# Kernel optimization log

Hardware: AMD Instinct MI355X
Metric: run time of the kernel (lower is better)

The kernel has to match this reference:

```python
import jax, jax.numpy as jnp
import numpy as np

B, N = 32, 512
NODE_F, EDGE_F = 64, 16
OUT = [64, 64, 64, 128]
TARGET = 16
DEGS = [1, 2, 3, 4]  # degree buckets (degree 0 filtered out, as in init_duvenaud)


def setup_inputs() -> dict:
    key = jax.random.key(0)
    ks = jax.random.split(key, 12)
    # adjacency: each node v connects to v+1..v+deg(v) (mod N), deg in {1..4}
    deg = jax.random.randint(ks[0], (B, N), 1, 5)
    off = jnp.arange(1, 5)                                   # (4,)
    cols = (jnp.arange(N)[:, None] + off[None, :]) % N       # (N,4)
    vals = (off[None, None, :] <= deg[:, :, None]).astype(jnp.float32)  # (B,N,4)
    g = jnp.zeros((B, N, N), jnp.float32).at[:, jnp.arange(N)[:, None], cols].set(vals)
    h_in = jax.random.normal(ks[1], (B, N, NODE_F), jnp.float32)
    e = jax.random.normal(ks[2], (B, N, N, EDGE_F), jnp.float32)
    # per-timestep, per-degree update matrices H_t: (n_deg, msg_in_t, out_t)
    ins = [NODE_F + EDGE_F, OUT[0] + EDGE_F, OUT[1] + EDGE_F]
    H0 = jax.random.normal(ks[3], (len(DEGS), ins[0], OUT[0]), jnp.float32)
    H1 = jax.random.normal(ks[4], (len(DEGS), ins[1], OUT[1]), jnp.float32)
    H2 = jax.random.normal(ks[5], (len(DEGS), ins[2], OUT[2]), jnp.float32)
    # readout matrices W_l for each of the 4 stored layers h^0..h^3
    layer_in = [NODE_F, OUT[0], OUT[1], OUT[2]]
    W0 = jax.random.normal(ks[6], (layer_in[0], OUT[3]), jnp.float32)
    W1 = jax.random.normal(ks[7], (layer_in[1], OUT[3]), jnp.float32)
    W2 = jax.random.normal(ks[8], (layer_in[2], OUT[3]), jnp.float32)
    W3 = jax.random.normal(ks[9], (layer_in[3], OUT[3]), jnp.float32)
    W_final = jax.random.normal(ks[10], (OUT[3], TARGET), jnp.float32) * 0.05
    b_final = jnp.zeros((TARGET,), jnp.float32)
    return {"g": g, "h_in": h_in, "e": e,
            "H0": H0, "H1": H1, "H2": H2,
            "W0": W0, "W1": W1, "W2": W2, "W3": W3,
            "W_final": W_final, "b_final": b_final}


def _step(g, e, h, H):
    # duvenaud message m_v = sum_w g[v,w] * cat(h_w, e_vw); split concat to avoid
    # materializing the (B,N,N,F+E) tensor the torch loop builds per node.
    mh = jnp.einsum('bvw,bwf->bvf', g, h)
    me = jnp.einsum('bvw,bvwe->bve', g, e)
    m = jnp.concatenate([mh, me], axis=-1)                 # (B,N,msg_in)
    deg = jnp.sum(g, axis=2)                               # (B,N) node degrees
    # degree-bucketed linear update: h'_v = m_v @ H[bucket(deg_v)]
    cand = jnp.einsum('bvm,dmo->bvdo', m, H)               # (B,N,n_deg,out)
    degs = jnp.asarray(DEGS, m.dtype)
    sel = (deg[:, :, None] == degs[None, None, :]).astype(m.dtype)  # one-hot bucket
    return jnp.einsum('bvd,bvdo->bvo', sel, cand)          # deg not in DEGS -> 0


def reference(g, h_in, e, H0, H1, H2, W0, W1, W2, W3, W_final, b_final):
    hs = [h_in]
    for H in (H0, H1, H2):
        hs.append(_step(g, e, hs[-1], H))
    # duvenaud readout: sum over layers/nodes of masked softmax(h_l @ W_l)
    acc = jnp.zeros((g.shape[0], W_final.shape[0]), h_in.dtype)
    for h, W in zip(hs, (W0, W1, W2, W3)):
        lin = jnp.einsum('bvf,fo->bvo', h, W)
        # mask rows whose linear output is all zero (padding / never-updated nodes)
        mask = (jnp.sum(lin != 0, axis=-1, keepdims=True) > 0).astype(lin.dtype)
        acc = acc + jnp.sum(jax.nn.softmax(lin, axis=-1) * mask, axis=1)
    out = acc @ W_final + b_final
    return jax.nn.softmax(out, axis=-1)
```

## Files before the change

kernel.cpp:

```cpp
#include <hip/hip_runtime.h>

#define BATCH 32
#define NN 512
#define NODE_F 64
#define EDGE_F 16
#define MSG 80
#define OUTF 64
#define RD 128
#define TGT 16
#define KMAX 8
#define ROWS (BATCH*NN)

__global__ __launch_bounds__(256) void preprocess_kernel(
    const float* __restrict__ g, const float* __restrict__ e,
    int* __restrict__ adj_idx, float* __restrict__ adj_val,
    int* __restrict__ nnzArr, int* __restrict__ bucketArr,
    float* __restrict__ me)
{
  __shared__ int   s_idx[4][KMAX];
  __shared__ float s_val[4][KMAX];
  int lane = threadIdx.x & 63;
  int wid  = threadIdx.x >> 6;
  int row  = blockIdx.x * 4 + wid;
  const float* grow = g + (size_t)row * NN;
  float deg = 0.f;
  int cnt = 0;
  for (int it = 0; it < NN/64; ++it) {
    int w = it*64 + lane;
    float gv = grow[w];
    deg += gv;
    unsigned long long m = __ballot(gv != 0.0f);
    int before = __popcll(m & ((1ull << lane) - 1ull));
    if (gv != 0.0f) {
      int pos = cnt + before;
      if (pos < KMAX) { s_idx[wid][pos] = w; s_val[wid][pos] = gv; }
    }
    cnt += __popcll(m);
  }
  for (int off = 32; off; off >>= 1) deg += __shfl_xor(deg, off);
  __syncthreads();
  const float* erow = e + (size_t)row * NN * EDGE_F;
  float mef = 0.f;
  if (cnt <= KMAX) {
    for (int k = 0; k < cnt; ++k) {
      int   wk = s_idx[wid][k];
      float vk = s_val[wid][k];
      if (lane < EDGE_F) mef += vk * erow[wk*EDGE_F + lane];
    }
  } else {
    for (int w = 0; w < NN; ++w) {
      float gv = grow[w];
      if (gv != 0.f && lane < EDGE_F) mef += gv * erow[w*EDGE_F + lane];
    }
  }
  if (lane < EDGE_F) me[(size_t)row*EDGE_F + lane] = mef;
  if (lane < KMAX && lane < cnt) {
    adj_idx[row*KMAX + lane] = s_idx[wid][lane];
    adj_val[row*KMAX + lane] = s_val[wid][lane];
  }
  if (lane == 0) {
    int bk = -1;
    if      (deg == 1.0f) bk = 0;
    else if (deg == 2.0f) bk = 1;
    else if (deg == 3.0f) bk = 2;
    else if (deg == 4.0f) bk = 3;
    bucketArr[row] = bk;
    nnzArr[row] = cnt;
  }
}

__global__ void scatter_kernel(const int* __restrict__ bucketArr,
                               int* __restrict__ counts, int* __restrict__ perm)
{
  int i = blockIdx.x * blockDim.x + threadIdx.x;
  if (i < ROWS) {
    int bk = bucketArr[i];
    if (bk >= 0) {
      int p = atomicAdd(&counts[bk], 1);
      perm[bk*ROWS + p] = i;
    }
  }
}

__global__ __launch_bounds__(256) void step_kernel(
    const float* __restrict__ h_prev, float* __restrict__ h_out,
    const float* __restrict__ Ht,
    const int* __restrict__ perm, const int* __restrict__ counts,
    const int* __restrict__ nnzArr, const int* __restrict__ adj_idx,
    const float* __restrict__ adj_val, const float* __restrict__ me,
    const float* __restrict__ g)
{
  int d = blockIdx.x >> 10;
  int chunk = blockIdx.x & 1023;
  int cnt = counts[d];
  int base = chunk * 16;
  if (base >= cnt) return;
  __shared__ float sm[16][MSG];
  __shared__ int   srow[16];
  int lane = threadIdx.x & 63;
  int wid  = threadIdx.x >> 6;
  for (int j = 0; j < 4; ++j) {
    int nl = wid + 4*j;
    int gi = base + nl;
    if (gi < cnt) {
      int row = perm[d*ROWS + gi];
      if (lane == 0) srow[nl] = row;
      int bb  = row >> 9;
      int nnz = nnzArr[row];
      float mh = 0.f;
      if (nnz <= KMAX) {
        for (int k = 0; k < nnz; ++k) {
          int   w  = adj_idx[row*KMAX + k];
          float vv = adj_val[row*KMAX + k];
          mh += vv * h_prev[((size_t)(bb*NN + w))*NODE_F + lane];
        }
      } else {
        const float* grow = g + (size_t)row * NN;
        for (int w = 0; w < NN; ++w) {
          float gv = grow[w];
          if (gv != 0.f) mh += gv * h_prev[((size_t)(bb*NN + w))*NODE_F + lane];
        }
      }
      sm[nl][lane] = mh;
      if (lane < EDGE_F) sm[nl][NODE_F + lane] = me[(size_t)row*EDGE_F + lane];
    } else {
      if (lane == 0) srow[nl] = -1;
      sm[nl][lane] = 0.f;
      if (lane < EDGE_F) sm[nl][NODE_F + lane] = 0.f;
    }
  }
  __syncthreads();
  const float* Hd = Ht + d * MSG * OUTF;
  int o = lane, q = wid;
  float a0=0.f, a1=0.f, a2=0.f, a3=0.f;
  for (int i = 0; i < MSG; ++i) {
    float hv = Hd[i*OUTF + o];
    a0 += sm[q   ][i]*hv;
    a1 += sm[q+ 4][i]*hv;
    a2 += sm[q+ 8][i]*hv;
    a3 += sm[q+12][i]*hv;
  }
  float av[4] = {a0,a1,a2,a3};
  for (int j = 0; j < 4; ++j) {
    int r = srow[q + 4*j];
    if (r >= 0) h_out[(size_t)r*OUTF + o] = av[j];
  }
}

__global__ __launch_bounds__(128) void readout_kernel(
    const float* __restrict__ h0, const float* __restrict__ h1,
    const float* __restrict__ h2, const float* __restrict__ h3,
    const float* __restrict__ W0, const float* __restrict__ W1,
    const float* __restrict__ W2, const float* __restrict__ W3,
    float* __restrict__ accv)
{
  int l = blockIdx.x >> 9;
  int chunk = blockIdx.x & 511;
  const float* hs = (l==0)?h0:(l==1)?h1:(l==2)?h2:h3;
  const float* Wl = (l==0)?W0:(l==1)?W1:(l==2)?W2:W3;
  __shared__ float sW[NODE_F*RD];
  __shared__ float sh[32*NODE_F];
  __shared__ float sred[2], sred2[2];
  __shared__ int   sflag[2];
  int tid = threadIdx.x;
  const float4* W4 = (const float4*)Wl;
  float4* sW4 = (float4*)sW;
  for (int i = tid; i < NODE_F*RD/4; i += 128) sW4[i] = W4[i];
  const float4* h4 = (const float4*)(hs + (size_t)chunk*32*NODE_F);
  float4* sh4 = (float4*)sh;
  for (int i = tid; i < 32*NODE_F/4; i += 128) sh4[i] = h4[i];
  __syncthreads();
  int o = tid, wid = tid >> 6, lane = tid & 63;
  int b = chunk >> 4;
  float accl = 0.f;
  for (int n = 0; n < 32; ++n) {
    float lin = 0.f;
    for (int i = 0; i < NODE_F; ++i) lin += sh[n*NODE_F+i] * sW[i*RD+o];
    float mx = lin;
    for (int off = 32; off; off >>= 1) mx = fmaxf(mx, __shfl_xor(mx, off));
    int anyw = (__ballot(lin != 0.f) != 0ull) ? 1 : 0;
    if (lane == 0) { sred[wid] = mx; sflag[wid] = anyw; }
    __syncthreads();
    mx = fmaxf(sred[0], sred[1]);
    int any = sflag[0] | sflag[1];
    float p = expf(lin - mx);
    float s = p;
    for (int off = 32; off; off >>= 1) s += __shfl_xor(s, off);
    if (lane == 0) sred2[wid] = s;
    __syncthreads();
    s = sred2[0] + sred2[1];
    if (any) accl += p / s;
    __syncthreads();
  }
  atomicAdd(&accv[b*RD + o], accl);
}

__global__ __launch_bounds__(512) void final_kernel(
    const float* __restrict__ accv, const float* __restrict__ Wf,
    const float* __restrict__ bf, float* __restrict__ out)
{
  int tid = threadIdx.x;
  int b = tid >> 4, t = tid & 15;
  float v = bf[t];
  for (int i = 0; i < RD; ++i) v += accv[b*RD + i] * Wf[i*TGT + t];
  float mx = v;
  for (int off = 8; off; off >>= 1) mx = fmaxf(mx, __shfl_xor(mx, off, 16));
  float p = expf(v - mx);
  float s = p;
  for (int off = 8; off; off >>= 1) s += __shfl_xor(s, off, 16);
  out[tid] = p / s;
}

extern "C" void kernel_launch(void* const* d_in, const int* in_sizes, int n_in,
                              void* d_out, int out_size, void* d_ws, size_t ws_size,
                              hipStream_t stream)
{
  const float* g    = (const float*)d_in[0];
  const float* h_in = (const float*)d_in[1];
  const float* e    = (const float*)d_in[2];
  const float* H0   = (const float*)d_in[3];
  const float* H1   = (const float*)d_in[4];
  const float* H2   = (const float*)d_in[5];
  const float* W0   = (const float*)d_in[6];
  const float* W1   = (const float*)d_in[7];
  const float* W2   = (const float*)d_in[8];
  const float* W3   = (const float*)d_in[9];
  const float* Wf   = (const float*)d_in[10];
  const float* bf   = (const float*)d_in[11];
  float* out = (float*)d_out;

  char* base = (char*)d_ws;
  size_t off = 0;
  auto alloc = [&](size_t bytes) -> void* {
    void* p = base + off;
    off = (off + bytes + 255) & ~(size_t)255;
    return p;
  };
  int*   adj_idx   = (int*)  alloc((size_t)ROWS*KMAX*sizeof(int));
  float* adj_val   = (float*)alloc((size_t)ROWS*KMAX*sizeof(float));
  int*   nnzArr    = (int*)  alloc((size_t)ROWS*sizeof(int));
  int*   bucketArr = (int*)  alloc((size_t)ROWS*sizeof(int));
  float* me        = (float*)alloc((size_t)ROWS*EDGE_F*sizeof(float));
  int*   perm      = (int*)  alloc((size_t)4*ROWS*sizeof(int));
  int*   counts    = (int*)  alloc(4*sizeof(int) + (size_t)BATCH*RD*sizeof(float));
  float* accv      = (float*)(counts + 4);
  float* h1        = (float*)alloc((size_t)ROWS*NODE_F*sizeof(float)*3);
  float* h2 = h1 + (size_t)ROWS*NODE_F;
  float* h3 = h2 + (size_t)ROWS*NODE_F;

  hipMemsetAsync(counts, 0, 4*sizeof(int) + (size_t)BATCH*RD*sizeof(float), stream);
  hipMemsetAsync(h1, 0, (size_t)ROWS*NODE_F*sizeof(float)*3, stream);

  preprocess_kernel<<<ROWS/4, 256, 0, stream>>>(g, e, adj_idx, adj_val, nnzArr, bucketArr, me);
  scatter_kernel<<<(ROWS+255)/256, 256, 0, stream>>>(bucketArr, counts, perm);
  step_kernel<<<4*1024, 256, 0, stream>>>(h_in, h1, H0, perm, counts, nnzArr, adj_idx, adj_val, me, g);
  step_kernel<<<4*1024, 256, 0, stream>>>(h1,   h2, H1, perm, counts, nnzArr, adj_idx, adj_val, me, g);
  step_kernel<<<4*1024, 256, 0, stream>>>(h2,   h3, H2, perm, counts, nnzArr, adj_idx, adj_val, me, g);
  readout_kernel<<<4*512, 128, 0, stream>>>(h_in, h1, h2, h3, W0, W1, W2, W3, accv);
  final_kernel<<<1, 512, 0, stream>>>(accv, Wf, bf, out);
}
```

Measured before the change: 903.2 us.

## Register-tile step and readout GEMMs with shared-memory staged weights

The step kernel now processes 64 nodes per block, stages the degree's H matrix in shared memory and computes a 4x4 register tile per thread from a transposed message buffer. The readout kernel handles 64 nodes per block with a 4x8 register tile and replaces the per-node barrier-heavy softmax with a block-wide two-pass reduction. The final kernel is split across one block per batch. The aim is to cut redundant global loads and per-node synchronisation, at the cost of more shared memory and registers per block.

```diff
diff --git a/kernel.cpp b/kernel.cpp
--- a/kernel.cpp
+++ b/kernel.cpp
@@ -90,27 +90,33 @@
     const float* __restrict__ adj_val, const float* __restrict__ me,
     const float* __restrict__ g)
 {
-  int d = blockIdx.x >> 10;
-  int chunk = blockIdx.x & 1023;
+  int d = blockIdx.x >> 8;
+  int chunk = blockIdx.x & 255;
   int cnt = counts[d];
-  int base = chunk * 16;
+  int base = chunk * 64;
   if (base >= cnt) return;
-  __shared__ float sm[16][MSG];
-  __shared__ int   srow[16];
-  int lane = threadIdx.x & 63;
-  int wid  = threadIdx.x >> 6;
-  for (int j = 0; j < 4; ++j) {
-    int nl = wid + 4*j;
+  __shared__ float smt[MSG][68];
+  __shared__ float sH[MSG*OUTF];
+  __shared__ int   srow[64];
+  int tid = threadIdx.x;
+  int lane = tid & 63, wid = tid >> 6;
+  {
+    const float4* H4 = (const float4*)(Ht + (size_t)d*MSG*OUTF);
+    float4* s4 = (float4*)sH;
+    for (int f = tid; f < MSG*OUTF/4; f += 256) s4[f] = H4[f];
+  }
+  for (int t = 0; t < 16; ++t) {
+    int nl = wid*16 + t;
     int gi = base + nl;
+    float mh = 0.f;
+    int row = -1;
     if (gi < cnt) {
-      int row = perm[d*ROWS + gi];
-      if (lane == 0) srow[nl] = row;
-      int bb  = row >> 9;
+      row = perm[d*ROWS + gi];
+      int bb = row >> 9;
       int nnz = nnzArr[row];
-      float mh = 0.f;
       if (nnz <= KMAX) {
         for (int k = 0; k < nnz; ++k) {
-          int   w  = adj_idx[row*KMAX + k];
+          int w = adj_idx[row*KMAX + k];
           float vv = adj_val[row*KMAX + k];
           mh += vv * h_prev[((size_t)(bb*NN + w))*NODE_F + lane];
         }
@@ -121,94 +127,190 @@
           if (gv != 0.f) mh += gv * h_prev[((size_t)(bb*NN + w))*NODE_F + lane];
         }
       }
-      sm[nl][lane] = mh;
-      if (lane < EDGE_F) sm[nl][NODE_F + lane] = me[(size_t)row*EDGE_F + lane];
-    } else {
-      if (lane == 0) srow[nl] = -1;
-      sm[nl][lane] = 0.f;
-      if (lane < EDGE_F) sm[nl][NODE_F + lane] = 0.f;
-    }
-  }
-  __syncthreads();
-  const float* Hd = Ht + d * MSG * OUTF;
-  int o = lane, q = wid;
-  float a0=0.f, a1=0.f, a2=0.f, a3=0.f;
+    }
+    smt[lane][nl] = mh;
+    if (lane < EDGE_F) smt[NODE_F + lane][nl] = (row >= 0) ? me[(size_t)row*EDGE_F + lane] : 0.f;
+    if (lane == 0) srow[nl] = row;
+  }
+  __syncthreads();
+  int tn = tid & 15, to = tid >> 4;
+  float4 acc[4];
+  acc[0] = acc[1] = acc[2] = acc[3] = make_float4(0.f,0.f,0.f,0.f);
+  #pragma unroll 8
   for (int i = 0; i < MSG; ++i) {
-    float hv = Hd[i*OUTF + o];
-    a0 += sm[q   ][i]*hv;
-    a1 += sm[q+ 4][i]*hv;
-    a2 += sm[q+ 8][i]*hv;
-    a3 += sm[q+12][i]*hv;
-  }
-  float av[4] = {a0,a1,a2,a3};
-  for (int j = 0; j < 4; ++j) {
-    int r = srow[q + 4*j];
-    if (r >= 0) h_out[(size_t)r*OUTF + o] = av[j];
-  }
-}
-
-__global__ __launch_bounds__(128) void readout_kernel(
+    float4 hv = *(const float4*)&smt[i][4*tn];
+    float4 wv = *(const float4*)&sH[i*OUTF + 4*to];
+    float hk[4] = {hv.x, hv.y, hv.z, hv.w};
+    #pragma unroll
+    for (int k = 0; k < 4; ++k) {
+      acc[k].x += hk[k]*wv.x; acc[k].y += hk[k]*wv.y;
+      acc[k].z += hk[k]*wv.z; acc[k].w += hk[k]*wv.w;
+    }
+  }
+  #pragma unroll
+  for (int k = 0; k < 4; ++k) {
+    int r = srow[4*tn + k];
+    if (r >= 0) *(float4*)&h_out[(size_t)r*OUTF + 4*to] = acc[k];
+  }
+}
+
+__global__ __launch_bounds__(256) void readout_kernel(
     const float* __restrict__ h0, const float* __restrict__ h1,
     const float* __restrict__ h2, const float* __restrict__ h3,
     const float* __restrict__ W0, const float* __restrict__ W1,
     const float* __restrict__ W2, const float* __restrict__ W3,
     float* __restrict__ accv)
 {
-  int l = blockIdx.x >> 9;
-  int chunk = blockIdx.x & 511;
+  int l = blockIdx.x >> 8;
+  int chunk = blockIdx.x & 255;
   const float* hs = (l==0)?h0:(l==1)?h1:(l==2)?h2:h3;
   const float* Wl = (l==0)?W0:(l==1)?W1:(l==2)?W2:W3;
   __shared__ float sW[NODE_F*RD];
-  __shared__ float sh[32*NODE_F];
-  __shared__ float sred[2], sred2[2];
-  __shared__ int   sflag[2];
+  __shared__ float sht[NODE_F*68];
+  __shared__ float snmax[64], snsum[64];
+  __shared__ int   snflag[64];
+  float* redm = sht;
+  int*   redf = (int*)(sht + 64*17);
   int tid = threadIdx.x;
-  const float4* W4 = (const float4*)Wl;
-  float4* sW4 = (float4*)sW;
-  for (int i = tid; i < NODE_F*RD/4; i += 128) sW4[i] = W4[i];
-  const float4* h4 = (const float4*)(hs + (size_t)chunk*32*NODE_F);
-  float4* sh4 = (float4*)sh;
-  for (int i = tid; i < 32*NODE_F/4; i += 128) sh4[i] = h4[i];
-  __syncthreads();
-  int o = tid, wid = tid >> 6, lane = tid & 63;
-  int b = chunk >> 4;
-  float accl = 0.f;
-  for (int n = 0; n < 32; ++n) {
-    float lin = 0.f;
-    for (int i = 0; i < NODE_F; ++i) lin += sh[n*NODE_F+i] * sW[i*RD+o];
-    float mx = lin;
-    for (int off = 32; off; off >>= 1) mx = fmaxf(mx, __shfl_xor(mx, off));
-    int anyw = (__ballot(lin != 0.f) != 0ull) ? 1 : 0;
-    if (lane == 0) { sred[wid] = mx; sflag[wid] = anyw; }
-    __syncthreads();
-    mx = fmaxf(sred[0], sred[1]);
-    int any = sflag[0] | sflag[1];
-    float p = expf(lin - mx);
-    float s = p;
-    for (int off = 32; off; off >>= 1) s += __shfl_xor(s, off);
-    if (lane == 0) sred2[wid] = s;
-    __syncthreads();
-    s = sred2[0] + sred2[1];
-    if (any) accl += p / s;
-    __syncthreads();
-  }
-  atomicAdd(&accv[b*RD + o], accl);
-}
-
-__global__ __launch_bounds__(512) void final_kernel(
+  {
+    const float4* W4 = (const float4*)Wl;
+    float4* sW4 = (float4*)sW;
+    #pragma unroll
+    for (int r = 0; r < 8; ++r) sW4[tid + 256*r] = W4[tid + 256*r];
+    const float4* hv4 = (const float4*)(hs + (size_t)chunk*64*NODE_F);
+    #pragma unroll
+    for (int r = 0; r < 4; ++r) {
+      int f = tid + 256*r;
+      int n = f >> 4, c = f & 15;
+      float4 v = hv4[f];
+      sht[(4*c+0)*68 + n] = v.x;
+      sht[(4*c+1)*68 + n] = v.y;
+      sht[(4*c+2)*68 + n] = v.z;
+      sht[(4*c+3)*68 + n] = v.w;
+    }
+  }
+  __syncthreads();
+  int tn = tid & 15, to = tid >> 4;
+  int b = chunk >> 3;
+  float4 accA[4], accB[4];
+  #pragma unroll
+  for (int k = 0; k < 4; ++k) { accA[k] = make_float4(0,0,0,0); accB[k] = make_float4(0,0,0,0); }
+  #pragma unroll 4
+  for (int i = 0; i < NODE_F; ++i) {
+    float4 hv = *(const float4*)&sht[i*68 + 4*tn];
+    float4 w0 = *(const float4*)&sW[i*128 + 8*to];
+    float4 w1 = *(const float4*)&sW[i*128 + 8*to + 4];
+    float hk[4] = {hv.x, hv.y, hv.z, hv.w};
+    #pragma unroll
+    for (int k = 0; k < 4; ++k) {
+      accA[k].x += hk[k]*w0.x; accA[k].y += hk[k]*w0.y;
+      accA[k].z += hk[k]*w0.z; accA[k].w += hk[k]*w0.w;
+      accB[k].x += hk[k]*w1.x; accB[k].y += hk[k]*w1.y;
+      accB[k].z += hk[k]*w1.z; accB[k].w += hk[k]*w1.w;
+    }
+  }
+  __syncthreads();
+  #pragma unroll
+  for (int k = 0; k < 4; ++k) {
+    float4 a = accA[k], bq = accB[k];
+    float pm = fmaxf(fmaxf(fmaxf(a.x,a.y),fmaxf(a.z,a.w)),
+                     fmaxf(fmaxf(bq.x,bq.y),fmaxf(bq.z,bq.w)));
+    int nz = (a.x!=0.f)||(a.y!=0.f)||(a.z!=0.f)||(a.w!=0.f)||
+             (bq.x!=0.f)||(bq.y!=0.f)||(bq.z!=0.f)||(bq.w!=0.f);
+    int n = 4*tn + k;
+    redm[n*17 + to] = pm;
+    redf[n*17 + to] = nz;
+  }
+  __syncthreads();
+  {
+    int n = tid >> 2, sub = tid & 3;
+    float m = redm[n*17 + sub*4 + 0];
+    m = fmaxf(m, redm[n*17 + sub*4 + 1]);
+    m = fmaxf(m, redm[n*17 + sub*4 + 2]);
+    m = fmaxf(m, redm[n*17 + sub*4 + 3]);
+    int f = redf[n*17 + sub*4 + 0] | redf[n*17 + sub*4 + 1] |
+            redf[n*17 + sub*4 + 2] | redf[n*17 + sub*4 + 3];
+    m = fmaxf(m, __shfl_xor(m, 1)); m = fmaxf(m, __shfl_xor(m, 2));
+    f |= __shfl_xor(f, 1); f |= __shfl_xor(f, 2);
+    if (sub == 0) { snmax[n] = m; snflag[n] = f; }
+  }
+  __syncthreads();
+  #pragma unroll
+  for (int k = 0; k < 4; ++k) {
+    int n = 4*tn + k;
+    float m = snmax[n];
+    accA[k].x = __expf(accA[k].x - m); accA[k].y = __expf(accA[k].y - m);
+    accA[k].z = __expf(accA[k].z - m); accA[k].w = __expf(accA[k].w - m);
+    accB[k].x = __expf(accB[k].x - m); accB[k].y = __expf(accB[k].y - m);
+    accB[k].z = __expf(accB[k].z - m); accB[k].w = __expf(accB[k].w - m);
+    float ps = accA[k].x+accA[k].y+accA[k].z+accA[k].w+
+               accB[k].x+accB[k].y+accB[k].z+accB[k].w;
+    redm[n*17 + to] = ps;
+  }
+  __syncthreads();
+  {
+    int n = tid >> 2, sub = tid & 3;
+    float s = redm[n*17 + sub*4 + 0] + redm[n*17 + sub*4 + 1] +
+              redm[n*17 + sub*4 + 2] + redm[n*17 + sub*4 + 3];
+    s += __shfl_xor(s, 1); s += __shfl_xor(s, 2);
+    if (sub == 0) snsum[n] = s;
+  }
+  __syncthreads();
+  float4 aj0 = make_float4(0,0,0,0), aj1 = make_float4(0,0,0,0);
+  #pragma unroll
+  for (int k = 0; k < 4; ++k) {
+    int n = 4*tn + k;
+    if (snflag[n]) {
+      float inv = 1.0f / snsum[n];
+      aj0.x += accA[k].x*inv; aj0.y += accA[k].y*inv;
+      aj0.z += accA[k].z*inv; aj0.w += accA[k].w*inv;
+      aj1.x += accB[k].x*inv; aj1.y += accB[k].y*inv;
+      aj1.z += accB[k].z*inv; aj1.w += accB[k].w*inv;
+    }
+  }
+  #pragma unroll
+  for (int off = 1; off < 16; off <<= 1) {
+    aj0.x += __shfl_xor(aj0.x, off); aj0.y += __shfl_xor(aj0.y, off);
+    aj0.z += __shfl_xor(aj0.z, off); aj0.w += __shfl_xor(aj0.w, off);
+    aj1.x += __shfl_xor(aj1.x, off); aj1.y += __shfl_xor(aj1.y, off);
+    aj1.z += __shfl_xor(aj1.z, off); aj1.w += __shfl_xor(aj1.w, off);
+  }
+  if (tn == 0) {
+    float* dst = &accv[b*RD + 8*to];
+    atomicAdd(dst+0, aj0.x); atomicAdd(dst+1, aj0.y);
+    atomicAdd(dst+2, aj0.z); atomicAdd(dst+3, aj0.w);
+    atomicAdd(dst+4, aj1.x); atomicAdd(dst+5, aj1.y);
+    atomicAdd(dst+6, aj1.z); atomicAdd(dst+7, aj1.w);
+  }
+}
+
+__global__ __launch_bounds__(256) void final_kernel(
     const float* __restrict__ accv, const float* __restrict__ Wf,
     const float* __restrict__ bf, float* __restrict__ out)
 {
+  int b = blockIdx.x;
   int tid = threadIdx.x;
-  int b = tid >> 4, t = tid & 15;
-  float v = bf[t];
-  for (int i = 0; i < RD; ++i) v += accv[b*RD + i] * Wf[i*TGT + t];
-  float mx = v;
-  for (int off = 8; off; off >>= 1) mx = fmaxf(mx, __shfl_xor(mx, off, 16));
-  float p = expf(v - mx);
-  float s = p;
-  for (int off = 8; off; off >>= 1) s += __shfl_xor(s, off, 16);
-  out[tid] = p / s;
+  int tg = tid & 15, part = tid >> 4;
+  float p = 0.f;
+  #pragma unroll
+  for (int q = 0; q < 8; ++q) {
+    int i = part*8 + q;
+    p += accv[b*RD + i] * Wf[i*TGT + tg];
+  }
+  __shared__ float pp[16][17];
+  pp[part][tg] = p;
+  __syncthreads();
+  if (tid < 16) {
+    float v = bf[tid];
+    #pragma unroll
+    for (int q = 0; q < 16; ++q) v += pp[q][tid];
+    float mx = v;
+    for (int off = 8; off; off >>= 1) mx = fmaxf(mx, __shfl_xor(mx, off, 16));
+    float e = __expf(v - mx);
+    float s = e;
+    for (int off = 8; off; off >>= 1) s += __shfl_xor(s, off, 16);
+    out[b*TGT + tid] = e / s;
+  }
 }
 
 extern "C" void kernel_launch(void* const* d_in, const int* in_sizes, int n_in,
@@ -252,10 +354,10 @@
   hipMemsetAsync(h1, 0, (size_t)ROWS*NODE_F*sizeof(float)*3, stream);
 
   preprocess_kernel<<<ROWS/4, 256, 0, stream>>>(g, e, adj_idx, adj_val, nnzArr, bucketArr, me);
-  scatter_kernel<<<(ROWS+255)/256, 256, 0, stream>>>(bucketArr, counts, perm);
-  step_kernel<<<4*1024, 256, 0, stream>>>(h_in, h1, H0, perm, counts, nnzArr, adj_idx, adj_val, me, g);
-  step_kernel<<<4*1024, 256, 0, stream>>>(h1,   h2, H1, perm, counts, nnzArr, adj_idx, adj_val, me, g);
-  step_kernel<<<4*1024, 256, 0, stream>>>(h2,   h3, H2, perm, counts, nnzArr, adj_idx, adj_val, me, g);
-  readout_kernel<<<4*512, 128, 0, stream>>>(h_in, h1, h2, h3, W0, W1, W2, W3, accv);
-  final_kernel<<<1, 512, 0, stream>>>(accv, Wf, bf, out);
-}
+  scatter_kernel<<<ROWS/256, 256, 0, stream>>>(bucketArr, counts, perm);
+  step_kernel<<<4*256, 256, 0, stream>>>(h_in, h1, H0, perm, counts, nnzArr, adj_idx, adj_val, me, g);
+  step_kernel<<<4*256, 256, 0, stream>>>(h1,   h2, H1, perm, counts, nnzArr, adj_idx, adj_val, me, g);
+  step_kernel<<<4*256, 256, 0, stream>>>(h2,   h3, H2, perm, counts, nnzArr, adj_idx, adj_val, me, g);
+  readout_kernel<<<4*256, 256, 0, stream>>>(h_in, h1, h2, h3, W0, W1, W2, W3, accv);
+  final_kernel<<<BATCH, 256, 0, stream>>>(accv, Wf, bf, out);
+}
```

After: 870.3 us. 3.6% less time.
